# Kernel optimization log

Measured on AMD Instinct MI355X. Metric: run time of the kernel, lower is better.

## Reference

```python
import jax, jax.numpy as jnp
import numpy as np

HID, H, KVH, D = 4096, 32, 8, 128  # hidden_size, attn heads, kv heads, head_dim

def _rms_norm(x, w, eps):
    # x: [B, S, h, D]; normalize over last dim (dim 3 in torch code)
    var = jnp.mean(jnp.square(x), axis=-1, keepdims=True)
    return x * jax.lax.rsqrt(var + eps) * w

def _rotate_half(x):
    x1, x2 = jnp.split(x, 2, axis=-1)
    return jnp.concatenate((-x2, x1), axis=-1)

def _rope(x, cos, sin):
    return x * cos + _rotate_half(x) * sin

def setup_inputs() -> dict:
    key = jax.random.key(0)
    ks = jax.random.split(key, 10)
    B, S = 1, 2048
    return {
        'hidden_states': jax.random.normal(ks[0], (B, S, HID), jnp.float32),
        'cos': jax.random.uniform(ks[1], (1, 1, S, D), jnp.float32, -1.0, 1.0),
        'sin': jax.random.uniform(ks[2], (1, 1, S, D), jnp.float32, -1.0, 1.0),
        'wq': jax.random.normal(ks[3], (HID, H * D), jnp.float32) * 0.02,
        'wk': jax.random.normal(ks[4], (HID, KVH * D), jnp.float32) * 0.02,
        'wv': jax.random.normal(ks[5], (HID, KVH * D), jnp.float32) * 0.02,
        'wo': jax.random.normal(ks[6], (H * D, HID), jnp.float32) * 0.02,
        'q_norm_w': jnp.ones((D,), jnp.float32),
        'k_norm_w': jnp.ones((D,), jnp.float32),
        'eps': jnp.float32(1e-6),
    }

def reference(hidden_states, cos, sin, wq, wk, wv, wo, q_norm_w, k_norm_w, eps):
    B, S, _ = hidden_states.shape
    n_rep = H // KVH
    # projections + per-head RMSNorm (before transpose, over head_dim)
    q = _rms_norm((hidden_states @ wq).reshape(B, S, H, D), q_norm_w, eps)
    k = _rms_norm((hidden_states @ wk).reshape(B, S, KVH, D), k_norm_w, eps)
    v = (hidden_states @ wv).reshape(B, S, KVH, D)
    q = q.transpose(0, 2, 1, 3)  # [B,H,S,D]
    k = k.transpose(0, 2, 1, 3)  # [B,KVH,S,D]
    v = v.transpose(0, 2, 1, 3)
    q, k = _rope(q, cos, sin), _rope(k, cos, sin)
    # GQA repeat (equivalent to repeat_interleave on head dim)
    k = jnp.repeat(k, n_rep, axis=1)
    v = jnp.repeat(v, n_rep, axis=1)
    # NOTE: source computes self.scaling but never applies it; no causal mask applied.
    attn = jnp.einsum('bhqd,bhkd->bhqk', q, k)
    attn = jax.nn.softmax(attn.astype(jnp.float32), axis=-1)
    out = jnp.einsum('bhqk,bhkd->bhqd', attn, v)
    out = out.transpose(0, 2, 1, 3).reshape(B, S, H * D)
    return out @ wo
```

## Files before the change

kernel.cpp:

```cpp
#include <hip/hip_runtime.h>
#include <hip/hip_bf16.h>
#include <stdint.h>

#define SLEN 2048
#define HIDN 4096
#define NHEAD 32
#define NKV 8
#define HD 128
#define QKV_N 6144

typedef __hip_bfloat16 bf16;
typedef short short8 __attribute__((ext_vector_type(8)));
typedef _Float16 f16x8 __attribute__((ext_vector_type(8)));
typedef float f32x4 __attribute__((ext_vector_type(4)));
typedef float f32x16 __attribute__((ext_vector_type(16)));

__device__ __forceinline__ void gld16(const void* g, void* l) {
  __builtin_amdgcn_global_load_lds((const __attribute__((address_space(1))) void*)g,
                                   (__attribute__((address_space(3))) void*)l,
                                   16, 0, 0);
}

__device__ __forceinline__ unsigned int cvtpk(float a, float b) {
  unsigned int r;
  asm("v_cvt_pk_bf16_f32 %0, %1, %2" : "=v"(r) : "v"(a), "v"(b));
  return r;
}

__global__ __launch_bounds__(256, 2) void gemm_pipe_kernel(
    const bf16* __restrict__ A, const bf16* __restrict__ B,
    float* __restrict__ C, int K, int lda, int ldb, int ldc)
{
  __shared__ __align__(16) bf16 sA[2][128 * 64];
  __shared__ __align__(16) bf16 sB[2][128 * 64];

  const int bidlin = blockIdx.y * gridDim.x + blockIdx.x;
  const int xcd = bidlin & 7;
  const int local = bidlin >> 3;
  const int CW = gridDim.x >> 2;
  const int cx = xcd & 3, cy = xcd >> 2;
  const int bx = cx * CW + local % CW;
  const int by = cy * (gridDim.y >> 1) + local / CW;
  const int row0 = by * 128;
  const int col0 = bx * 128;

  const int tid = threadIdx.x;
  const int w = tid >> 6;
  const int lane = tid & 63;
  const int wr = w >> 1, wc = w & 1;
  const int fr = lane & 15;
  const int g = lane >> 4;

  auto stage = [&](int t, int b) {
    const int k0 = t << 6;
#pragma unroll
    for (int i = 0; i < 4; ++i) {
      const int c = i * 256 + tid;
      const int row = c >> 3;
      const int slot = (c & 7) ^ (row & 7);
      gld16(A + (long)(row0 + row) * lda + k0 + slot * 8,
            (bf16*)sA[b] + (i * 256 + w * 64) * 8);
    }
#pragma unroll
    for (int i = 0; i < 4; ++i) {
      const int c = i * 256 + tid;
      const int row = c >> 3;
      const int slot = (c & 7) ^ (row & 7);
      gld16(B + (long)(col0 + row) * ldb + k0 + slot * 8,
            (bf16*)sB[b] + (i * 256 + w * 64) * 8);
    }
  };

  f32x4 acc[4][4] = {};
  const int nk = K >> 6;

  stage(0, 0);

  for (int t = 0; t < nk; ++t) {
    const int buf = t & 1;
    __builtin_amdgcn_s_barrier();
    __builtin_amdgcn_sched_barrier(0);
    if (t + 1 < nk) {
      stage(t + 1, buf ^ 1);
      asm volatile("s_waitcnt vmcnt(8)" ::: "memory");
    } else {
      asm volatile("s_waitcnt vmcnt(0)" ::: "memory");
    }
    __builtin_amdgcn_sched_barrier(0);
    __builtin_amdgcn_s_barrier();
    __builtin_amdgcn_sched_barrier(0);

    const bf16* Ab = sA[buf];
    const bf16* Bb = sB[buf];

    short8 afr[4][2], bfr[4][2];
#pragma unroll
    for (int mf = 0; mf < 4; ++mf)
#pragma unroll
      for (int ks = 0; ks < 2; ++ks) {
        const int ra = wr * 64 + mf * 16 + fr;
        afr[mf][ks] = *(const short8*)(Ab + ra * 64 + (((ks << 2) + g) ^ (ra & 7)) * 8);
        const int rb = wc * 64 + mf * 16 + fr;
        bfr[mf][ks] = *(const short8*)(Bb + rb * 64 + (((ks << 2) + g) ^ (rb & 7)) * 8);
      }
    __builtin_amdgcn_s_setprio(1);
#pragma unroll
    for (int mf = 0; mf < 4; ++mf)
#pragma unroll
      for (int nf = 0; nf < 4; ++nf)
#pragma unroll
        for (int ks = 0; ks < 2; ++ks)
          acc[mf][nf] = __builtin_amdgcn_mfma_f32_16x16x32_bf16(
              afr[mf][ks], bfr[nf][ks], acc[mf][nf], 0, 0, 0);
    __builtin_amdgcn_s_setprio(0);
  }

  const int cr = g << 2;
#pragma unroll
  for (int mf = 0; mf < 4; ++mf)
#pragma unroll
    for (int nf = 0; nf < 4; ++nf)
#pragma unroll
      for (int r = 0; r < 4; ++r) {
        const long row = row0 + wr * 64 + mf * 16 + cr + r;
        const long col = col0 + wc * 64 + nf * 16 + fr;
        C[row * (long)ldc + col] = acc[mf][nf][r];
      }
}

__global__ __launch_bounds__(256, 2) void gemm_qkv_kernel(
    const bf16* __restrict__ A, const bf16* __restrict__ B,
    _Float16* __restrict__ qf, _Float16* __restrict__ kf,
    bf16* __restrict__ Vt,
    const float* __restrict__ cosb, const float* __restrict__ sinb,
    const float* __restrict__ qw, const float* __restrict__ kw,
    const float* __restrict__ epsp, int K, int lda, int ldb)
{
  __shared__ __align__(16) char smem[128 * 133 * 4];
  bf16* sAb = (bf16*)smem;
  bf16* sBb = (bf16*)(smem + 32768);
  float* T = (float*)smem;

  const int bidlin = blockIdx.y * gridDim.x + blockIdx.x;
  const int xcd = bidlin & 7;
  const int local = bidlin >> 3;
  const int CW = gridDim.x >> 2;
  const int cx = xcd & 3, cy = xcd >> 2;
  const int bx = cx * CW + local % CW;
  const int by = cy * (gridDim.y >> 1) + local / CW;
  const int row0 = by * 128;
  const int col0 = bx * 128;

  const int tid = threadIdx.x;
  const int w = tid >> 6;
  const int lane = tid & 63;
  const int wr = w >> 1, wc = w & 1;
  const int fr = lane & 15;
  const int g = lane >> 4;

  auto stage = [&](int t, int b) {
    const int k0 = t << 6;
#pragma unroll
    for (int i = 0; i < 4; ++i) {
      const int c = i * 256 + tid;
      const int row = c >> 3;
      const int slot = (c & 7) ^ (row & 7);
      gld16(A + (long)(row0 + row) * lda + k0 + slot * 8,
            sAb + b * 8192 + (i * 256 + w * 64) * 8);
    }
#pragma unroll
    for (int i = 0; i < 4; ++i) {
      const int c = i * 256 + tid;
      const int row = c >> 3;
      const int slot = (c & 7) ^ (row & 7);
      gld16(B + (long)(col0 + row) * ldb + k0 + slot * 8,
            sBb + b * 8192 + (i * 256 + w * 64) * 8);
    }
  };

  f32x4 acc[4][4] = {};
  const int nk = K >> 6;

  stage(0, 0);

  for (int t = 0; t < nk; ++t) {
    const int buf = t & 1;
    __builtin_amdgcn_s_barrier();
    __builtin_amdgcn_sched_barrier(0);
    if (t + 1 < nk) {
      stage(t + 1, buf ^ 1);
      asm volatile("s_waitcnt vmcnt(8)" ::: "memory");
    } else {
      asm volatile("s_waitcnt vmcnt(0)" ::: "memory");
    }
    __builtin_amdgcn_sched_barrier(0);
    __builtin_amdgcn_s_barrier();
    __builtin_amdgcn_sched_barrier(0);

    const bf16* Ab = sAb + buf * 8192;
    const bf16* Bb = sBb + buf * 8192;

    short8 afr[4][2], bfr[4][2];
#pragma unroll
    for (int mf = 0; mf < 4; ++mf)
#pragma unroll
      for (int ks = 0; ks < 2; ++ks) {
        const int ra = wr * 64 + mf * 16 + fr;
        afr[mf][ks] = *(const short8*)(Ab + ra * 64 + (((ks << 2) + g) ^ (ra & 7)) * 8);
        const int rb = wc * 64 + mf * 16 + fr;
        bfr[mf][ks] = *(const short8*)(Bb + rb * 64 + (((ks << 2) + g) ^ (rb & 7)) * 8);
      }
    __builtin_amdgcn_s_setprio(1);
#pragma unroll
    for (int mf = 0; mf < 4; ++mf)
#pragma unroll
      for (int nf = 0; nf < 4; ++nf)
#pragma unroll
        for (int ks = 0; ks < 2; ++ks)
          acc[mf][nf] = __builtin_amdgcn_mfma_f32_16x16x32_bf16(
              afr[mf][ks], bfr[nf][ks], acc[mf][nf], 0, 0, 0);
    __builtin_amdgcn_s_setprio(0);
  }

  __syncthreads();
#pragma unroll
  for (int mf = 0; mf < 4; ++mf)
#pragma unroll
    for (int nf = 0; nf < 4; ++nf)
#pragma unroll
      for (int r = 0; r < 4; ++r)
        T[(wr * 64 + mf * 16 + (g << 2) + r) * 133 + wc * 64 + nf * 16 + fr] =
            acc[mf][nf][r];
  __syncthreads();

  const int slot = col0 >> 7;
  if (slot < 40) {
    const int rrow = w * 32 + (lane & 31);
    const int hi2 = lane >> 5;
    const long srow = row0 + rrow;
    const float* nw = (slot < 32) ? qw : kw;
    _Float16* dst;
    long base;
    float scale;
    if (slot < 32) {
      dst = qf; base = ((long)slot * SLEN + srow) * HD;
      scale = 1.4426950408889634f;
    } else {
      dst = kf; base = ((long)(slot - 32) * SLEN + srow) * HD;
      scale = 1.0f;
    }
    float ssq = 0.0f;
#pragma unroll
    for (int j = 0; j < 64; ++j) {
      const float v = T[rrow * 133 + hi2 * 64 + j];
      ssq += v * v;
    }
    ssq += __shfl_xor(ssq, 32);
    const float rr = rsqrtf(ssq * (1.0f / 128.0f) + epsp[0]);
#pragma unroll
    for (int jv = 0; jv < 8; ++jv) {
      f16x8 o8;
#pragma unroll
      for (int e = 0; e < 8; ++e) {
        const int d = hi2 * 64 + jv * 8 + e;
        const float nv  = T[rrow * 133 + d] * rr * nw[d];
        const float nvp = T[rrow * 133 + (d ^ 64)] * rr * nw[d ^ 64];
        const float c = cosb[srow * HD + d];
        const float s = sinb[srow * HD + d];
        const float ov = hi2 ? (nv * c + nvp * s) : (nv * c - nvp * s);
        o8[e] = (_Float16)(ov * scale);
      }
      *(f16x8*)(dst + base + hi2 * 64 + jv * 8) = o8;
    }
  } else {
    const int kvh = slot - 40;
    const int d = w * 32 + (lane >> 1);
    const int sh = lane & 1;
    const long vb = (long)kvh * HD * SLEN + (long)d * SLEN + row0 + sh * 64;
#pragma unroll
    for (int jv = 0; jv < 8; ++jv) {
      short8 o8;
#pragma unroll
      for (int e = 0; e < 8; ++e) {
        const bf16 hv = __float2bfloat16(T[(sh * 64 + jv * 8 + e) * 133 + d]);
        short sb;
        __builtin_memcpy(&sb, &hv, 2);
        o8[e] = sb;
      }
      *(short8*)(Vt + vb + jv * 8) = o8;
    }
  }
}

__global__ __launch_bounds__(256) void transpose_kernel(
    const float* __restrict__ src, long srcZ, int srcLd,
    bf16* __restrict__ dst, long dstZ, int dstLd)
{
  __shared__ float t[64][65];
  const int z = blockIdx.z;
  src += (long)z * srcZ;
  const long db = (long)z * dstZ;
  const int k0 = blockIdx.x * 64;
  const int n0 = blockIdx.y * 64;
  const int tx = threadIdx.x & 63;
  const int ty = threadIdx.x >> 6;
#pragma unroll
  for (int r = ty; r < 64; r += 4)
    t[r][tx] = src[(long)(k0 + r) * srcLd + n0 + tx];
  __syncthreads();
  const int tx2 = threadIdx.x & 31;
  const int ty2 = threadIdx.x >> 5;
#pragma unroll
  for (int r = ty2; r < 64; r += 8) {
    const unsigned int pr = cvtpk(t[2 * tx2][r], t[2 * tx2 + 1][r]);
    *(unsigned int*)(dst + db + (long)(n0 + r) * dstLd + k0 + 2 * tx2) = pr;
  }
}

__global__ __launch_bounds__(256) void cvt_bf16_kernel(
    const float* __restrict__ x, bf16* __restrict__ y, int n)
{
  const int i = (blockIdx.x * 256 + threadIdx.x) * 4;
  if (i >= n) return;
  const f32x4 v = *(const f32x4*)(x + i);
#pragma unroll
  for (int j = 0; j < 4; ++j) y[i + j] = __float2bfloat16(v[j]);
}

__global__ __launch_bounds__(256, 2) void flash_kernel(
    const _Float16* __restrict__ qf, const _Float16* __restrict__ kf,
    const bf16* __restrict__ vt,
    bf16* __restrict__ AO)
{
  __shared__ __align__(16) _Float16 sK[2][64 * 128];
  __shared__ __align__(16) bf16 sV[2][64 * 128];

  const int lin = blockIdx.x;
  const int swz = (lin & 7) * 64 + (lin >> 3);
  const int head = swz >> 4;
  const int qt = swz & 15;
  const int kvh = head >> 2;

  const int tid = threadIdx.x;
  const int w = tid >> 6;
  const int lane = tid & 63;
  const int q31 = lane & 31;
  const int hi = lane >> 5;

  f16x8 bq[8];
  {
    const long qb = ((long)head * SLEN + qt * 128 + w * 32 + q31) * HD + hi * 8;
#pragma unroll
    for (int ks = 0; ks < 8; ++ks)
      bq[ks] = *(const f16x8*)(qf + qb + ks * 16);
  }

  short8 ones;
#pragma unroll
  for (int e = 0; e < 8; ++e) ones[e] = (short)0x3F80;

  const _Float16* kb = kf + (long)kvh * SLEN * HD;
  const bf16* vb = vt + (long)kvh * HD * SLEN;

  auto stage = [&](int t, int buf) {
#pragma unroll
    for (int i = 0; i < 4; ++i) {
      const int c = i * 256 + tid;
      const int row = c >> 4;
      const int sg = (c & 15) ^ (row & 15);
      gld16(kb + (long)(t * 64 + row) * HD + sg * 8,
            (_Float16*)sK[buf] + (i * 256 + w * 64) * 8);
    }
#pragma unroll
    for (int i = 0; i < 4; ++i) {
      const int c = i * 256 + tid;
      const int rp = c >> 4;
      const int sg = (c & 15) ^ (rp & 15);
      const int d = rp * 2 + (sg >> 3);
      gld16(vb + (long)d * SLEN + t * 64 + (sg & 7) * 8,
            (bf16*)sV[buf] + (i * 256 + w * 64) * 8);
    }
  };

  f32x16 o[4] = {};
  f32x16 o4 = {};

  stage(0, 0);
  stage(1, 1);
  asm volatile("s_waitcnt vmcnt(8)" ::: "memory");
  __builtin_amdgcn_sched_barrier(0);
  __builtin_amdgcn_s_barrier();
  __builtin_amdgcn_sched_barrier(0);

  for (int t = 0; t < SLEN / 64; ++t) {
    const int cur = t & 1;
    const _Float16* K = sK[cur];
    const bf16* V = sV[cur];

    f32x16 s0 = {}, s1 = {};
    __builtin_amdgcn_s_setprio(1);
#pragma unroll
    for (int ks = 0; ks < 8; ++ks) {
      const int slot = (2 * ks + hi) ^ (q31 & 15);
      const f16x8 a0 = *(const f16x8*)(K + q31 * 128 + slot * 8);
      const f16x8 a1 = *(const f16x8*)(K + (32 + q31) * 128 + slot * 8);
      s0 = __builtin_amdgcn_mfma_f32_32x32x16_f16(a0, bq[ks], s0, 0, 0, 0);
      s1 = __builtin_amdgcn_mfma_f32_32x32x16_f16(a1, bq[ks], s1, 0, 0, 0);
    }
    __builtin_amdgcn_s_setprio(0);

#pragma unroll
    for (int r = 0; r < 16; ++r) s0[r] = exp2f(s0[r]);
#pragma unroll
    for (int r = 0; r < 16; ++r) s1[r] = exp2f(s1[r]);

    unsigned int pk[16], sw[16];
#pragma unroll
    for (int i = 0; i < 8; ++i) pk[i] = cvtpk(s0[2 * i], s0[2 * i + 1]);
#pragma unroll
    for (int i = 0; i < 8; ++i) pk[8 + i] = cvtpk(s1[2 * i], s1[2 * i + 1]);
#pragma unroll
    for (int i = 0; i < 16; ++i) sw[i] = __shfl_xor((int)pk[i], 32);

    short8 pa[4];
#pragma unroll
    for (int ks = 0; ks < 4; ++ks) {
      const int base = (ks >> 1) * 8 + (ks & 1) * 4 + 2 * hi;
      union { unsigned int u[4]; short8 v; } tu;
      if (hi == 0) {
        tu.u[0] = pk[base]; tu.u[1] = pk[base + 1];
        tu.u[2] = sw[base]; tu.u[3] = sw[base + 1];
      } else {
        tu.u[0] = sw[base]; tu.u[1] = sw[base + 1];
        tu.u[2] = pk[base]; tu.u[3] = pk[base + 1];
      }
      pa[ks] = tu.v;
    }

    __builtin_amdgcn_s_setprio(1);
#pragma unroll
    for (int ks = 0; ks < 4; ++ks)
      o4 = __builtin_amdgcn_mfma_f32_32x32x16_bf16(pa[ks], ones, o4, 0, 0, 0);
#pragma unroll
    for (int nt = 0; nt < 4; ++nt) {
      const int d = nt * 32 + q31;
      const int rp = d >> 1;
      const int sbase = ((d & 1) << 3) + hi;
#pragma unroll
      for (int ks = 0; ks < 4; ++ks) {
        const int slot = (sbase + 2 * ks) ^ (rp & 15);
        const short8 bv = *(const short8*)(V + rp * 128 + slot * 8);
        o[nt] = __builtin_amdgcn_mfma_f32_32x32x16_bf16(pa[ks], bv, o[nt], 0, 0, 0);
      }
    }
    __builtin_amdgcn_s_setprio(0);

    __builtin_amdgcn_s_barrier();
    __builtin_amdgcn_sched_barrier(0);
    if (t + 2 < SLEN / 64) {
      stage(t + 2, cur);
      asm volatile("s_waitcnt vmcnt(8)" ::: "memory");
    } else {
      asm volatile("s_waitcnt vmcnt(0)" ::: "memory");
    }
    __builtin_amdgcn_sched_barrier(0);
    __builtin_amdgcn_s_barrier();
    __builtin_amdgcn_sched_barrier(0);
  }

  f32x16 inv;
#pragma unroll
  for (int r = 0; r < 16; ++r) inv[r] = 1.0f / o4[r];
#pragma unroll
  for (int nt = 0; nt < 4; ++nt)
#pragma unroll
    for (int rr = 0; rr < 4; ++rr)
#pragma unroll
      for (int j = 0; j < 4; ++j) {
        const long row = qt * 128 + w * 32 + 8 * rr + 4 * hi + j;
        AO[row * HIDN + head * 128 + nt * 32 + q31] =
            __float2bfloat16(o[nt][rr * 4 + j] * inv[rr * 4 + j]);
      }
}

extern "C" void kernel_launch(void* const* d_in, const int* in_sizes, int n_in,
                              void* d_out, int out_size, void* d_ws, size_t ws_size,
                              hipStream_t stream)
{
  const float* hs   = (const float*)d_in[0];
  const float* cosb = (const float*)d_in[1];
  const float* sinb = (const float*)d_in[2];
  const float* wq   = (const float*)d_in[3];
  const float* wk   = (const float*)d_in[4];
  const float* wv   = (const float*)d_in[5];
  const float* wo   = (const float*)d_in[6];
  const float* qw   = (const float*)d_in[7];
  const float* kw   = (const float*)d_in[8];
  const float* eps  = (const float*)d_in[9];

  const size_t MB = 1024 * 1024;
  if (ws_size < 116 * MB) return;
  uint8_t* ws = (uint8_t*)d_ws;

  bf16*  hsb = (bf16*)(ws + 0 * MB);
  bf16*  WT  = (bf16*)(ws + 16 * MB);
  _Float16* qf = (_Float16*)(ws + 64 * MB);
  _Float16* kf = (_Float16*)(ws + 80 * MB);
  bf16*  Vt  = (bf16*)(ws + 84 * MB);
  bf16*  AO  = (bf16*)(ws + 88 * MB);
  bf16*  WoT = (bf16*)(ws + 0 * MB);

  cvt_bf16_kernel<<<SLEN * HIDN / 4 / 256, 256, 0, stream>>>(hs, hsb, SLEN * HIDN);

  transpose_kernel<<<dim3(64, 64, 1), 256, 0, stream>>>(wq, 0, HIDN, WT, 0, HIDN);
  transpose_kernel<<<dim3(64, 16, 1), 256, 0, stream>>>(wk, 0, 1024, WT + (size_t)4096 * HIDN, 0, HIDN);
  transpose_kernel<<<dim3(64, 16, 1), 256, 0, stream>>>(wv, 0, 1024, WT + (size_t)5120 * HIDN, 0, HIDN);

  gemm_qkv_kernel<<<dim3(48, 16, 1), 256, 0, stream>>>(
      hsb, WT, qf, kf, Vt, cosb, sinb, qw, kw, eps, HIDN, HIDN, HIDN);

  transpose_kernel<<<dim3(64, 64, 1), 256, 0, stream>>>(wo, 0, HIDN, WoT, 0, HIDN);

  flash_kernel<<<dim3(512, 1, 1), 256, 0, stream>>>(qf, kf, Vt, AO);

  gemm_pipe_kernel<<<dim3(32, 16, 1), 256, 0, stream>>>(AO, WoT, (float*)d_out, HIDN, HIDN, HIDN, HIDN);
}
```

Baseline: 386.8 us.

## Shrink QKV GEMM LDS footprint to raise occupancy with register-side RMSNorm epilogue

Halves the K-tile of the QKV projection GEMM from 64 to 32, which halves the double-buffered LDS staging, and raises launch bounds from 2 to 3 blocks per CU. The epilogue now computes the RMSNorm sum of squares directly from accumulator registers, using shuffles plus a small cross-wave stat array. It stages bf16/f16 values in a 16-bit LDS tile instead of a full fp32 tile, so the epilogue fits in the smaller shared buffer. Risks include more loop iterations and barriers per K step, tighter register limits under the higher occupancy bound, and the rotate-half partner now being read back as bf16, which slightly changes precision.

```diff
diff --git a/kernel.cpp b/kernel.cpp
--- a/kernel.cpp
+++ b/kernel.cpp
@@ -128,7 +128,7 @@
       }
 }
 
-__global__ __launch_bounds__(256, 2) void gemm_qkv_kernel(
+__global__ __launch_bounds__(256, 3) void gemm_qkv_kernel(
     const bf16* __restrict__ A, const bf16* __restrict__ B,
     _Float16* __restrict__ qf, _Float16* __restrict__ kf,
     bf16* __restrict__ Vt,
@@ -136,10 +136,11 @@
     const float* __restrict__ qw, const float* __restrict__ kw,
     const float* __restrict__ epsp, int K, int lda, int ldb)
 {
-  __shared__ __align__(16) char smem[128 * 133 * 4];
+  __shared__ __align__(16) char smem[35840];
   bf16* sAb = (bf16*)smem;
-  bf16* sBb = (bf16*)(smem + 32768);
-  float* T = (float*)smem;
+  bf16* sBb = (bf16*)(smem + 16384);
+  unsigned short* T16 = (unsigned short*)smem;
+  float* stat = (float*)(smem + 34816);
 
   const int bidlin = blockIdx.y * gridDim.x + blockIdx.x;
   const int xcd = bidlin & 7;
@@ -159,27 +160,27 @@
   const int g = lane >> 4;
 
   auto stage = [&](int t, int b) {
-    const int k0 = t << 6;
-#pragma unroll
-    for (int i = 0; i < 4; ++i) {
+    const int k0 = t << 5;
+#pragma unroll
+    for (int i = 0; i < 2; ++i) {
       const int c = i * 256 + tid;
-      const int row = c >> 3;
-      const int slot = (c & 7) ^ (row & 7);
+      const int row = c >> 2;
+      const int slot = (c & 3) ^ (row & 3);
       gld16(A + (long)(row0 + row) * lda + k0 + slot * 8,
-            sAb + b * 8192 + (i * 256 + w * 64) * 8);
-    }
-#pragma unroll
-    for (int i = 0; i < 4; ++i) {
+            sAb + b * 4096 + (i * 256 + w * 64) * 8);
+    }
+#pragma unroll
+    for (int i = 0; i < 2; ++i) {
       const int c = i * 256 + tid;
-      const int row = c >> 3;
-      const int slot = (c & 7) ^ (row & 7);
+      const int row = c >> 2;
+      const int slot = (c & 3) ^ (row & 3);
       gld16(B + (long)(col0 + row) * ldb + k0 + slot * 8,
-            sBb + b * 8192 + (i * 256 + w * 64) * 8);
+            sBb + b * 4096 + (i * 256 + w * 64) * 8);
     }
   };
 
   f32x4 acc[4][4] = {};
-  const int nk = K >> 6;
+  const int nk = K >> 5;
 
   stage(0, 0);
 
@@ -189,7 +190,7 @@
     __builtin_amdgcn_sched_barrier(0);
     if (t + 1 < nk) {
       stage(t + 1, buf ^ 1);
-      asm volatile("s_waitcnt vmcnt(8)" ::: "memory");
+      asm volatile("s_waitcnt vmcnt(4)" ::: "memory");
     } else {
       asm volatile("s_waitcnt vmcnt(0)" ::: "memory");
     }
@@ -197,82 +198,150 @@
     __builtin_amdgcn_s_barrier();
     __builtin_amdgcn_sched_barrier(0);
 
-    const bf16* Ab = sAb + buf * 8192;
-    const bf16* Bb = sBb + buf * 8192;
-
-    short8 afr[4][2], bfr[4][2];
-#pragma unroll
-    for (int mf = 0; mf < 4; ++mf)
-#pragma unroll
-      for (int ks = 0; ks < 2; ++ks) {
-        const int ra = wr * 64 + mf * 16 + fr;
-        afr[mf][ks] = *(const short8*)(Ab + ra * 64 + (((ks << 2) + g) ^ (ra & 7)) * 8);
-        const int rb = wc * 64 + mf * 16 + fr;
-        bfr[mf][ks] = *(const short8*)(Bb + rb * 64 + (((ks << 2) + g) ^ (rb & 7)) * 8);
-      }
+    const bf16* Ab = sAb + buf * 4096;
+    const bf16* Bb = sBb + buf * 4096;
+
+    short8 afr[4], bfr[4];
+#pragma unroll
+    for (int mf = 0; mf < 4; ++mf) {
+      const int ra = wr * 64 + mf * 16 + fr;
+      afr[mf] = *(const short8*)(Ab + ra * 32 + (g ^ (ra & 3)) * 8);
+      const int rb = wc * 64 + mf * 16 + fr;
+      bfr[mf] = *(const short8*)(Bb + rb * 32 + (g ^ (rb & 3)) * 8);
+    }
     __builtin_amdgcn_s_setprio(1);
 #pragma unroll
     for (int mf = 0; mf < 4; ++mf)
 #pragma unroll
       for (int nf = 0; nf < 4; ++nf)
-#pragma unroll
-        for (int ks = 0; ks < 2; ++ks)
-          acc[mf][nf] = __builtin_amdgcn_mfma_f32_16x16x32_bf16(
-              afr[mf][ks], bfr[nf][ks], acc[mf][nf], 0, 0, 0);
+        acc[mf][nf] = __builtin_amdgcn_mfma_f32_16x16x32_bf16(
+            afr[mf], bfr[nf], acc[mf][nf], 0, 0, 0);
     __builtin_amdgcn_s_setprio(0);
   }
 
   __syncthreads();
-#pragma unroll
-  for (int mf = 0; mf < 4; ++mf)
-#pragma unroll
-    for (int nf = 0; nf < 4; ++nf)
-#pragma unroll
-      for (int r = 0; r < 4; ++r)
-        T[(wr * 64 + mf * 16 + (g << 2) + r) * 133 + wc * 64 + nf * 16 + fr] =
-            acc[mf][nf][r];
-  __syncthreads();
-
   const int slot = col0 >> 7;
+  const int cr = g << 2;
+
   if (slot < 40) {
+    float ssqp[4][4];
+#pragma unroll
+    for (int mf = 0; mf < 4; ++mf)
+#pragma unroll
+      for (int r = 0; r < 4; ++r) {
+        float s = 0.0f;
+#pragma unroll
+        for (int nf = 0; nf < 4; ++nf) s += acc[mf][nf][r] * acc[mf][nf][r];
+        s += __shfl_xor(s, 1);
+        s += __shfl_xor(s, 2);
+        s += __shfl_xor(s, 4);
+        s += __shfl_xor(s, 8);
+        ssqp[mf][r] = s;
+      }
+    if (fr == 0) {
+#pragma unroll
+      for (int mf = 0; mf < 4; ++mf)
+#pragma unroll
+        for (int r = 0; r < 4; ++r)
+          stat[(wr * 64 + mf * 16 + cr + r) * 2 + wc] = ssqp[mf][r];
+    }
+    __syncthreads();
+
+    const float epsv = epsp[0];
+    const float scale = (slot < 32) ? 1.4426950408889634f : 1.0f;
+    const float* nw = (slot < 32) ? qw : kw;
+    float nwv[4];
+#pragma unroll
+    for (int nf = 0; nf < 4; ++nf) nwv[nf] = nw[wc * 64 + nf * 16 + fr];
+
+    float rrv[4][4];
+#pragma unroll
+    for (int mf = 0; mf < 4; ++mf)
+#pragma unroll
+      for (int r = 0; r < 4; ++r) {
+        const int row = wr * 64 + mf * 16 + cr + r;
+        rrv[mf][r] = rsqrtf((stat[row * 2] + stat[row * 2 + 1]) * (1.0f / 128.0f) + epsv);
+      }
+
+    float nv[4][4][4];
+#pragma unroll
+    for (int mf = 0; mf < 4; ++mf)
+#pragma unroll
+      for (int nf = 0; nf < 4; ++nf)
+#pragma unroll
+        for (int r = 0; r < 4; ++r) {
+          const float v = acc[mf][nf][r] * rrv[mf][r] * nwv[nf];
+          nv[mf][nf][r] = v;
+          const int row = wr * 64 + mf * 16 + cr + r;
+          const int col = wc * 64 + nf * 16 + fr;
+          const bf16 hv = __float2bfloat16(v);
+          unsigned short ub;
+          __builtin_memcpy(&ub, &hv, 2);
+          T16[row * 136 + col] = ub;
+        }
+    __syncthreads();
+
+    unsigned short ofp[4][4][4];
+#pragma unroll
+    for (int mf = 0; mf < 4; ++mf)
+#pragma unroll
+      for (int nf = 0; nf < 4; ++nf)
+#pragma unroll
+        for (int r = 0; r < 4; ++r) {
+          const int row = wr * 64 + mf * 16 + cr + r;
+          const int col = wc * 64 + nf * 16 + fr;
+          const long srow = row0 + row;
+          unsigned short pb = T16[row * 136 + (col ^ 64)];
+          bf16 pbh;
+          __builtin_memcpy(&pbh, &pb, 2);
+          const float nvp = __bfloat162float(pbh);
+          const float c = cosb[srow * HD + col];
+          const float s = sinb[srow * HD + col];
+          const float ov = (wc == 0) ? (nv[mf][nf][r] * c - nvp * s)
+                                     : (nv[mf][nf][r] * c + nvp * s);
+          const _Float16 oh = (_Float16)(ov * scale);
+          unsigned short ob;
+          __builtin_memcpy(&ob, &oh, 2);
+          ofp[mf][nf][r] = ob;
+        }
+    __syncthreads();
+#pragma unroll
+    for (int mf = 0; mf < 4; ++mf)
+#pragma unroll
+      for (int nf = 0; nf < 4; ++nf)
+#pragma unroll
+        for (int r = 0; r < 4; ++r) {
+          const int row = wr * 64 + mf * 16 + cr + r;
+          const int col = wc * 64 + nf * 16 + fr;
+          T16[row * 136 + col] = ofp[mf][nf][r];
+        }
+    __syncthreads();
+
+    _Float16* dst = (slot < 32) ? qf : kf;
+    const int hidx = (slot < 32) ? slot : (slot - 32);
     const int rrow = w * 32 + (lane & 31);
     const int hi2 = lane >> 5;
-    const long srow = row0 + rrow;
-    const float* nw = (slot < 32) ? qw : kw;
-    _Float16* dst;
-    long base;
-    float scale;
-    if (slot < 32) {
-      dst = qf; base = ((long)slot * SLEN + srow) * HD;
-      scale = 1.4426950408889634f;
-    } else {
-      dst = kf; base = ((long)(slot - 32) * SLEN + srow) * HD;
-      scale = 1.0f;
-    }
-    float ssq = 0.0f;
-#pragma unroll
-    for (int j = 0; j < 64; ++j) {
-      const float v = T[rrow * 133 + hi2 * 64 + j];
-      ssq += v * v;
-    }
-    ssq += __shfl_xor(ssq, 32);
-    const float rr = rsqrtf(ssq * (1.0f / 128.0f) + epsp[0]);
+    const long base = ((long)hidx * SLEN + row0 + rrow) * HD;
 #pragma unroll
     for (int jv = 0; jv < 8; ++jv) {
-      f16x8 o8;
-#pragma unroll
-      for (int e = 0; e < 8; ++e) {
-        const int d = hi2 * 64 + jv * 8 + e;
-        const float nv  = T[rrow * 133 + d] * rr * nw[d];
-        const float nvp = T[rrow * 133 + (d ^ 64)] * rr * nw[d ^ 64];
-        const float c = cosb[srow * HD + d];
-        const float s = sinb[srow * HD + d];
-        const float ov = hi2 ? (nv * c + nvp * s) : (nv * c - nvp * s);
-        o8[e] = (_Float16)(ov * scale);
-      }
+      const f16x8 o8 = *(const f16x8*)((const _Float16*)T16 + rrow * 136 + hi2 * 64 + jv * 8);
       *(f16x8*)(dst + base + hi2 * 64 + jv * 8) = o8;
     }
   } else {
+#pragma unroll
+    for (int mf = 0; mf < 4; ++mf)
+#pragma unroll
+      for (int nf = 0; nf < 4; ++nf)
+#pragma unroll
+        for (int r = 0; r < 4; ++r) {
+          const int row = wr * 64 + mf * 16 + cr + r;
+          const int col = wc * 64 + nf * 16 + fr;
+          const bf16 hv = __float2bfloat16(acc[mf][nf][r]);
+          unsigned short ub;
+          __builtin_memcpy(&ub, &hv, 2);
+          T16[row * 136 + col] = ub;
+        }
+    __syncthreads();
     const int kvh = slot - 40;
     const int d = w * 32 + (lane >> 1);
     const int sh = lane & 1;
@@ -281,12 +350,8 @@
     for (int jv = 0; jv < 8; ++jv) {
       short8 o8;
 #pragma unroll
-      for (int e = 0; e < 8; ++e) {
-        const bf16 hv = __float2bfloat16(T[(sh * 64 + jv * 8 + e) * 133 + d]);
-        short sb;
-        __builtin_memcpy(&sb, &hv, 2);
-        o8[e] = sb;
-      }
+      for (int e = 0; e < 8; ++e)
+        o8[e] = (short)T16[(sh * 64 + jv * 8 + e) * 136 + d];
       *(short8*)(Vt + vb + jv * 8) = o8;
     }
   }
```

After: 398.2 us. 1.03x slower.

## Single-buffer V tile in flash kernel to fit three blocks per CU

Applied to the files above, without the earlier changes.

Cuts V shared-memory staging from two buffers to one, dropping LDS per block from 64KB to 48KB, and raises launch bounds from 2 to 3 blocks per SM. The prefetch schedule is reorganised so V for the next tile is loaded after the PV MMAs, and an extra wait plus barrier sits before the PV phase. More resident blocks are meant to hide latency better, but V loads are now exposed inside each iteration and the tighter register cap may cause spills.

```diff
diff --git a/kernel.cpp b/kernel.cpp
--- a/kernel.cpp
+++ b/kernel.cpp
@@ -327,13 +327,13 @@
   for (int j = 0; j < 4; ++j) y[i + j] = __float2bfloat16(v[j]);
 }
 
-__global__ __launch_bounds__(256, 2) void flash_kernel(
+__global__ __launch_bounds__(256, 3) void flash_kernel(
     const _Float16* __restrict__ qf, const _Float16* __restrict__ kf,
     const bf16* __restrict__ vt,
     bf16* __restrict__ AO)
 {
   __shared__ __align__(16) _Float16 sK[2][64 * 128];
-  __shared__ __align__(16) bf16 sV[2][64 * 128];
+  __shared__ __align__(16) bf16 sV[64 * 128];
 
   const int lin = blockIdx.x;
   const int swz = (lin & 7) * 64 + (lin >> 3);
@@ -362,7 +362,7 @@
   const _Float16* kb = kf + (long)kvh * SLEN * HD;
   const bf16* vb = vt + (long)kvh * HD * SLEN;
 
-  auto stage = [&](int t, int buf) {
+  auto stageK = [&](int t, int buf) {
 #pragma unroll
     for (int i = 0; i < 4; ++i) {
       const int c = i * 256 + tid;
@@ -371,6 +371,8 @@
       gld16(kb + (long)(t * 64 + row) * HD + sg * 8,
             (_Float16*)sK[buf] + (i * 256 + w * 64) * 8);
     }
+  };
+  auto stageV = [&](int t) {
 #pragma unroll
     for (int i = 0; i < 4; ++i) {
       const int c = i * 256 + tid;
@@ -378,24 +380,25 @@
       const int sg = (c & 15) ^ (rp & 15);
       const int d = rp * 2 + (sg >> 3);
       gld16(vb + (long)d * SLEN + t * 64 + (sg & 7) * 8,
-            (bf16*)sV[buf] + (i * 256 + w * 64) * 8);
+            (bf16*)sV + (i * 256 + w * 64) * 8);
     }
   };
 
   f32x16 o[4] = {};
   f32x16 o4 = {};
 
-  stage(0, 0);
-  stage(1, 1);
+  stageK(0, 0);
+  stageV(0);
+  stageK(1, 1);
   asm volatile("s_waitcnt vmcnt(8)" ::: "memory");
   __builtin_amdgcn_sched_barrier(0);
   __builtin_amdgcn_s_barrier();
   __builtin_amdgcn_sched_barrier(0);
 
-  for (int t = 0; t < SLEN / 64; ++t) {
+  const int NT = SLEN / 64;
+  for (int t = 0; t < NT; ++t) {
     const int cur = t & 1;
     const _Float16* K = sK[cur];
-    const bf16* V = sV[cur];
 
     f32x16 s0 = {}, s1 = {};
     __builtin_amdgcn_s_setprio(1);
@@ -437,6 +440,15 @@
       pa[ks] = tu.v;
     }
 
+    if (t + 1 < NT) {
+      asm volatile("s_waitcnt vmcnt(4)" ::: "memory");
+    } else {
+      asm volatile("s_waitcnt vmcnt(0)" ::: "memory");
+    }
+    __builtin_amdgcn_sched_barrier(0);
+    __builtin_amdgcn_s_barrier();
+    __builtin_amdgcn_sched_barrier(0);
+
     __builtin_amdgcn_s_setprio(1);
 #pragma unroll
     for (int ks = 0; ks < 4; ++ks)
@@ -449,23 +461,24 @@
 #pragma unroll
       for (int ks = 0; ks < 4; ++ks) {
         const int slot = (sbase + 2 * ks) ^ (rp & 15);
-        const short8 bv = *(const short8*)(V + rp * 128 + slot * 8);
+        const short8 bv = *(const short8*)((const bf16*)sV + rp * 128 + slot * 8);
         o[nt] = __builtin_amdgcn_mfma_f32_32x32x16_bf16(pa[ks], bv, o[nt], 0, 0, 0);
       }
     }
     __builtin_amdgcn_s_setprio(0);
 
-    __builtin_amdgcn_s_barrier();
-    __builtin_amdgcn_sched_barrier(0);
-    if (t + 2 < SLEN / 64) {
-      stage(t + 2, cur);
-      asm volatile("s_waitcnt vmcnt(8)" ::: "memory");
-    } else {
-      asm volatile("s_waitcnt vmcnt(0)" ::: "memory");
-    }
-    __builtin_amdgcn_sched_barrier(0);
-    __builtin_amdgcn_s_barrier();
-    __builtin_amdgcn_sched_barrier(0);
+    if (t + 1 < NT) {
+      __builtin_amdgcn_s_barrier();
+      __builtin_amdgcn_sched_barrier(0);
+      stageV(t + 1);
+      const bool ik = (t + 2 < NT);
+      if (ik) stageK(t + 2, cur);
+      if (ik) { asm volatile("s_waitcnt vmcnt(8)" ::: "memory"); }
+      else    { asm volatile("s_waitcnt vmcnt(4)" ::: "memory"); }
+      __builtin_amdgcn_sched_barrier(0);
+      __builtin_amdgcn_s_barrier();
+      __builtin_amdgcn_sched_barrier(0);
+    }
   }
 
   f32x16 inv;
```

Result: slower. 774.7 us (+100.3%).
